# Optimization experiments

Hardware: AMD Instinct MI355X
Metric: run time of the kernel (lower is better)

## Reference

```python
import jax, jax.numpy as jnp
import numpy as np

N_CG_ITERS = 100


def _conv_same(x, k):
    # x: [C,H,W], k: [kh,kw]; depthwise cross-correlation, zero padding ('same')
    C = x.shape[0]
    rhs = jnp.broadcast_to(k, (C, 1) + k.shape)  # [C,1,kh,kw]
    return jax.lax.conv_general_dilated(
        x[None], rhs, window_strides=(1, 1), padding='SAME',
        dimension_numbers=('NCHW', 'OIHW', 'NCHW'),
        feature_group_count=C)[0]


def _flip(k):
    return k[::-1, ::-1]


def _apply_A(p, kernel, wsq, reg_kernels):
    # A = K^T K + sum_i w_i^2 G_i^T G_i
    KtKp = _conv_same(_conv_same(p, kernel), _flip(kernel))
    def one_reg(g):
        return _conv_same(_conv_same(p, g), _flip(g))
    reg = jax.vmap(one_reg)(reg_kernels)  # [n_reg, C, H, W]
    return KtKp + jnp.einsum('n,nchw->chw', wsq, reg)


def setup_inputs() -> dict:
    key = jax.random.key(0)
    k1, k2, k3, k4 = jax.random.split(key, 4)
    image = jax.random.uniform(k1, (3, 512, 512), dtype=jnp.float32)
    kernel = jax.random.uniform(k2, (11, 11), dtype=jnp.float32)
    kernel = kernel / jnp.sum(kernel)  # normalized blur PSF
    reg_kernels = 0.01 * jax.random.normal(k3, (2, 3, 3), dtype=jnp.float32)
    reg_kernel_weights = 1.0 + 0.01 * jax.random.normal(k4, (2,), dtype=jnp.float32)
    return {'image': image, 'kernel': kernel,
            'reg_kernel_weights': reg_kernel_weights, 'reg_kernels': reg_kernels}


def reference(image, kernel, reg_kernel_weights, reg_kernels):
    wsq = reg_kernel_weights * reg_kernel_weights
    # CG init: b = K^T * image, x0 = image, r0 = b - A x0, p0 = r0
    b = _conv_same(image, _flip(kernel))
    x0 = image
    r0 = b - _apply_A(x0, kernel, wsq, reg_kernels)
    p0 = r0

    def cg_step(carry, _):
        x, r, p = carry
        Ap = _apply_A(p, kernel, wsq, reg_kernels)
        rTr = jnp.sum(r * r)
        alpha = rTr / jnp.sum(p * Ap)
        x_new = x + alpha * p
        r_new = r - alpha * Ap
        beta = jnp.sum(r_new * r_new) / rTr
        p_new = r_new + beta * p
        return (x_new, r_new, p_new), None

    (x, r, p), _ = jax.lax.scan(cg_step, (x0, r0, p0), None, length=N_CG_ITERS)
    return x  # xrp[0] -> solved image [C,H,W]
```

## Files before the change

### kernel.cpp

```cpp
#include <hip/hip_runtime.h>


static constexpr int H = 512, W = 512, CCH = 3;
static constexpr int TDIM = 64;
static constexpr int RAD = 5;
static constexpr int HALO = 10;
static constexpr int PR = TDIM + 2 * HALO;
static constexpr int PSTR = 84;
static constexpr int TR = TDIM + 2 * RAD;
static constexpr int TSTR = 76;
static constexpr int NBLK = CCH * 8 * 8;
static constexpr int NTHR = 512;
static constexpr int NITER = 100;
static constexpr int FRN = 2960;
static constexpr int SPN = 2160;

__device__ __forceinline__ void load18(const float* __restrict__ row, float* __restrict__ v)
{
    const float4 a = *reinterpret_cast<const float4*>(row + 0);
    const float4 b = *reinterpret_cast<const float4*>(row + 4);
    const float4 c = *reinterpret_cast<const float4*>(row + 8);
    const float4 d = *reinterpret_cast<const float4*>(row + 12);
    const float2 e = *reinterpret_cast<const float2*>(row + 16);
    v[0]=a.x; v[1]=a.y; v[2]=a.z; v[3]=a.w;
    v[4]=b.x; v[5]=b.y; v[6]=b.z; v[7]=b.w;
    v[8]=c.x; v[9]=c.y; v[10]=c.z; v[11]=c.w;
    v[12]=d.x; v[13]=d.y; v[14]=d.z; v[15]=d.w;
    v[16]=e.x; v[17]=e.y;
}

__device__ __forceinline__ float2 allreduce2_bar(unsigned long long* slots, unsigned seq,
                                                 float va, float vb,
                                                 float* redA, float* redB, float2* bc,
                                                 int tid, int bid)
{
    __syncthreads();
    #pragma unroll
    for (int m = 32; m; m >>= 1) { va += __shfl_xor(va, m, 64); vb += __shfl_xor(vb, m, 64); }
    if ((tid & 63) == 0) { redA[tid >> 6] = va; redB[tid >> 6] = vb; }
    asm volatile("s_waitcnt vmcnt(0)" ::: "memory");
    __syncthreads();
    unsigned long long* bufA = slots + (size_t)(seq & 1u) * 512;
    unsigned long long* bufB = bufA + 256;
    if (tid == 0) {
        float sa = 0.f, sb = 0.f;
        #pragma unroll
        for (int i = 0; i < NTHR / 64; ++i) { sa += redA[i]; sb += redB[i]; }
        __hip_atomic_store(&bufA[bid],
            ((unsigned long long)seq << 32) | (unsigned long long)__float_as_uint(sa),
            __ATOMIC_RELAXED, __HIP_MEMORY_SCOPE_AGENT);
        __hip_atomic_store(&bufB[bid],
            ((unsigned long long)seq << 32) | (unsigned long long)__float_as_uint(sb),
            __ATOMIC_RELAXED, __HIP_MEMORY_SCOPE_AGENT);
    }
    float ma = 0.f, mb = 0.f;
    if (tid < NBLK) {
        unsigned long long v;
        for (;;) {
            v = __hip_atomic_load(&bufA[tid], __ATOMIC_RELAXED, __HIP_MEMORY_SCOPE_AGENT);
            if ((unsigned)(v >> 32) == seq) break;
            __builtin_amdgcn_s_sleep(1);
        }
        ma = __uint_as_float((unsigned)v);
        for (;;) {
            v = __hip_atomic_load(&bufB[tid], __ATOMIC_RELAXED, __HIP_MEMORY_SCOPE_AGENT);
            if ((unsigned)(v >> 32) == seq) break;
            __builtin_amdgcn_s_sleep(1);
        }
        mb = __uint_as_float((unsigned)v);
    }
    __syncthreads();
    #pragma unroll
    for (int m = 32; m; m >>= 1) { ma += __shfl_xor(ma, m, 64); mb += __shfl_xor(mb, m, 64); }
    if ((tid & 63) == 0) { redA[tid >> 6] = ma; redB[tid >> 6] = mb; }
    __syncthreads();
    if (tid == 0) {
        float sa = 0.f, sb = 0.f;
        #pragma unroll
        for (int i = 0; i < NTHR / 64; ++i) { sa += redA[i]; sb += redB[i]; }
        bc->x = sa; bc->y = sb;
    }
    __syncthreads();
    return *bc;
}

__device__ __forceinline__ void conv_fwd_phase(const float* __restrict__ kern,
                                               const float* __restrict__ P_,
                                               float* __restrict__ T_,
                                               int by0, int bx0, int tid)
{
    for (int seg = tid; seg < TR * 10; seg += NTHR) {
        int chunk = seg / TR;
        int ry    = seg - chunk * TR;
        int rx0   = chunk << 3;
        int gy    = by0 - RAD + ry;
        bool rowIn = (gy >= 0 && gy < H);
        float acc[8];
        #pragma unroll
        for (int j = 0; j < 8; ++j) acc[j] = 0.f;
        for (int a = 0; a < 11; ++a) {
            float v[18];
            load18(P_ + (ry + a) * PSTR + rx0, v);
            #pragma unroll
            for (int b = 0; b < 11; ++b) {
                float kw = kern[a * 11 + b];
                #pragma unroll
                for (int j = 0; j < 8; ++j) acc[j] = fmaf(v[b + j], kw, acc[j]);
            }
        }
        #pragma unroll
        for (int j = 0; j < 8; ++j) {
            int gx = bx0 - RAD + rx0 + j;
            bool in = rowIn && gx >= 0 && gx < W;
            acc[j] = in ? acc[j] : 0.f;
        }
        float* dst = T_ + ry * TSTR + rx0;
        if (rx0 < 72) {
            *reinterpret_cast<float4*>(dst)     = make_float4(acc[0], acc[1], acc[2], acc[3]);
            *reinterpret_cast<float4*>(dst + 4) = make_float4(acc[4], acc[5], acc[6], acc[7]);
        } else {
            dst[0] = acc[0];
            dst[1] = acc[1];
        }
    }
}

__device__ __forceinline__ void conv11_flip_acc_v(const float* __restrict__ src, int stride,
                                                  int row0, int col0,
                                                  const float* __restrict__ kern,
                                                  float acc[8])
{
    for (int a = 0; a < 11; ++a) {
        float v[18];
        load18(src + (row0 + a) * stride + col0, v);
        #pragma unroll
        for (int b = 0; b < 11; ++b) {
            float kw = kern[(10 - a) * 11 + (10 - b)];
            #pragma unroll
            for (int j = 0; j < 8; ++j) acc[j] = fmaf(v[b + j], kw, acc[j]);
        }
    }
}

__device__ __forceinline__ void conv11_flip_acc_s(const float* __restrict__ src, int stride,
                                                  int row0, int col0,
                                                  const float* __restrict__ kern,
                                                  float acc[8])
{
    for (int a = 0; a < 11; ++a) {
        const float* row = src + (row0 + a) * stride + col0;
        float v[18];
        #pragma unroll
        for (int b = 0; b < 18; ++b) v[b] = row[b];
        #pragma unroll
        for (int b = 0; b < 11; ++b) {
            float kw = kern[(10 - a) * 11 + (10 - b)];
            #pragma unroll
            for (int j = 0; j < 8; ++j) acc[j] = fmaf(v[b + j], kw, acc[j]);
        }
    }
}

__device__ __forceinline__ void reg_uniform(const float* __restrict__ P_,
                                            const float* __restrict__ CB_,
                                            const float* __restrict__ gk,
                                            float w0sq, float w1sq,
                                            int oy, int ox0, int gy, int gx0,
                                            float acc[8])
{
    for (int a = 0; a < 5; ++a) {
        const float* row = P_ + (oy + 8 + a) * PSTR + ox0 + 8;
        const float4 q0 = *reinterpret_cast<const float4*>(row);
        const float4 q1 = *reinterpret_cast<const float4*>(row + 4);
        const float4 q2 = *reinterpret_cast<const float4*>(row + 8);
        float v[12] = {q0.x,q0.y,q0.z,q0.w, q1.x,q1.y,q1.z,q1.w, q2.x,q2.y,q2.z,q2.w};
        #pragma unroll
        for (int b = 0; b < 5; ++b) {
            float cb = CB_[a * 5 + b];
            #pragma unroll
            for (int j = 0; j < 8; ++j) acc[j] = fmaf(v[b + j], cb, acc[j]);
        }
    }
    if (!(gy > 0 && gy < H - 1 && gx0 > 0 && gx0 + 7 < W - 1)) {
        for (int j = 0; j < 8; ++j) {
            int gx = gx0 + j;
            if (gy > 0 && gy < H - 1 && gx > 0 && gx < W - 1) continue;
            float corr = 0.f;
            for (int dy = -1; dy <= 1; ++dy)
                for (int dx = -1; dx <= 1; ++dx) {
                    int qy = gy + dy, qx = gx + dx;
                    if (qy >= 0 && qy < H && qx >= 0 && qx < W) continue;
                    float u0 = 0.f, u1 = 0.f;
                    int pr0 = oy + HALO + dy - 1, pc0 = ox0 + j + HALO + dx - 1;
                    for (int sy = 0; sy < 3; ++sy)
                        for (int sx = 0; sx < 3; ++sx) {
                            float pv = P_[(pr0 + sy) * PSTR + pc0 + sx];
                            u0 = fmaf(pv, gk[sy * 3 + sx], u0);
                            u1 = fmaf(pv, gk[9 + sy * 3 + sx], u1);
                        }
                    corr += w0sq * gk[(1 - dy) * 3 + (1 - dx)] * u0
                          + w1sq * gk[9 + (1 - dy) * 3 + (1 - dx)] * u1;
                }
            acc[j] -= corr;
        }
    }
}

__global__ void slot_init(unsigned long long* slots) { slots[threadIdx.x] = 0ull; }

__global__ void __launch_bounds__(NTHR)
deconv_cg(const float* __restrict__ img, const float* __restrict__ kern,
          const float* __restrict__ wts, const float* __restrict__ gk,
          float* __restrict__ out, float* __restrict__ ws)
{
    __shared__ alignas(16) float P[PR * PSTR + 8];
    __shared__ alignas(16) float T[TR * TSTR + 8];
    __shared__ float Sf[FRN];
    __shared__ float CB[25];
    __shared__ float redA[NTHR / 64], redB[NTHR / 64];
    __shared__ float2 bc2;

    const int tid = threadIdx.x;
    const int bid = blockIdx.x;
    const int ch  = bid / 64;
    const int tt  = bid - ch * 64;
    const int by0 = (tt >> 3) * TDIM;
    const int bx0 = (tt & 7) * TDIM;

    const float* imgc = img + ch * H * W;
    unsigned long long* slots = (unsigned long long*)ws;
    float* Hc = ws + 2048 + (size_t)ch * H * W;

    const float w0 = wts[0], w1 = wts[1];
    const float w0sq = w0 * w0, w1sq = w1 * w1;

    if (tid < 25) {
        int ty = tid / 5 - 2, tx = tid % 5 - 2;
        float s = 0.f;
        for (int ay = 0; ay < 3; ++ay)
            for (int ax = 0; ax < 3; ++ax) {
                int by_ = ay + ty, bx_ = ax + tx;
                if (by_ >= 0 && by_ < 3 && bx_ >= 0 && bx_ < 3)
                    s += w0sq * gk[ay * 3 + ax] * gk[by_ * 3 + bx_]
                       + w1sq * gk[9 + ay * 3 + ax] * gk[9 + by_ * 3 + bx_];
            }
        CB[tid] = s;
    }

    const int oy  = tid & 63;
    const int ox0 = (tid >> 6) << 3;
    const int gy  = by0 + oy;
    const int gx0 = bx0 + ox0;

    int fP[6], fG[6], fS[6];
    #pragma unroll
    for (int k = 0; k < 6; ++k) {
        int idx = tid + k * NTHR;
        fP[k] = -1; fG[k] = -1; fS[k] = idx;
        if (idx < FRN) {
            int py, px;
            if (idx < 840)       { py = idx / 84;              px = idx - py * 84; }
            else if (idx < 1680) { int t = idx - 840;  py = 74 + t / 84; px = t - (t / 84) * 84; }
            else                 { int t = idx - 1680; py = 10 + t / 20;
                                   int c = t - (t / 20) * 20;  px = (c < 10) ? c : (c + 64); }
            int iy = by0 - HALO + py, ix = bx0 - HALO + px;
            if (iy >= 0 && iy < H && ix >= 0 && ix < W) {
                fP[k] = py * PSTR + px;
                fG[k] = iy * W + ix;
            }
        }
    }
    int pT[5], pG[5];
    #pragma unroll
    for (int k = 0; k < 5; ++k) {
        int idx = tid + k * NTHR;
        pT[k] = -1; pG[k] = 0;
        if (idx < SPN) {
            int sy, sx;
            if (idx < 640)       { sy = idx >> 6;              sx = idx & 63; }
            else if (idx < 1280) { int t = idx - 640;  sy = 54 + (t >> 6); sx = t & 63; }
            else                 { int t = idx - 1280; sy = 10 + t / 20;
                                   int c = t - (t / 20) * 20;  sx = (c < 10) ? c : (c + 44); }
            pT[k] = sy * TSTR + sx;
            pG[k] = (by0 + sy) * W + bx0 + sx;
        }
    }

    float xr[8], rr[8], pr[8], sr[8];
    #pragma unroll
    for (int j = 0; j < 8; ++j) { pr[j] = 0.f; sr[j] = 0.f; }
    for (int idx = tid; idx < FRN; idx += NTHR) Sf[idx] = 0.f;

    for (int idx = tid; idx < PR * PR; idx += NTHR) {
        int py = idx / PR, px = idx - py * PR;
        int iy = by0 - HALO + py, ix = bx0 - HALO + px;
        float v = 0.f;
        if (iy >= 0 && iy < H && ix >= 0 && ix < W) v = imgc[iy * W + ix];
        P[py * PSTR + px] = v;
    }
    __syncthreads();
    conv_fwd_phase(kern, P, T, by0, bx0, tid);
    __syncthreads();
    {
        float accA[8], accB[8];
        #pragma unroll
        for (int j = 0; j < 8; ++j) { accA[j] = 0.f; accB[j] = 0.f; }
        conv11_flip_acc_v(T, TSTR, oy, ox0, kern, accA);
        conv11_flip_acc_s(P, PSTR, oy + 5, ox0 + 5, kern, accB);
        reg_uniform(P, CB, gk, w0sq, w1sq, oy, ox0, gy, gx0, accA);
        #pragma unroll
        for (int j = 0; j < 8; ++j) {
            rr[j] = accB[j] - accA[j];
            xr[j] = P[(oy + HALO) * PSTR + ox0 + HALO + j];
        }
        __syncthreads();
        float* st = T + oy * TSTR + ox0;
        *reinterpret_cast<float4*>(st)     = make_float4(rr[0], rr[1], rr[2], rr[3]);
        *reinterpret_cast<float4*>(st + 4) = make_float4(rr[4], rr[5], rr[6], rr[7]);
        __syncthreads();
        #pragma unroll
        for (int k = 0; k < 5; ++k)
            if (pT[k] >= 0)
                __hip_atomic_store(&Hc[pG[k]], T[pT[k]],
                                   __ATOMIC_RELAXED, __HIP_MEMORY_SCOPE_AGENT);
        (void)allreduce2_bar(slots, 1u, 0.f, 0.f, redA, redB, &bc2, tid, bid);
        #pragma unroll
        for (int k = 0; k < 6; ++k)
            if (fG[k] >= 0)
                P[fP[k]] = __hip_atomic_load(&Hc[fG[k]],
                                             __ATOMIC_RELAXED, __HIP_MEMORY_SCOPE_AGENT);
        float* ow = P + (oy + HALO) * PSTR + ox0 + HALO;
        *reinterpret_cast<float2*>(ow)     = make_float2(rr[0], rr[1]);
        *reinterpret_cast<float2*>(ow + 2) = make_float2(rr[2], rr[3]);
        *reinterpret_cast<float2*>(ow + 4) = make_float2(rr[4], rr[5]);
        *reinterpret_cast<float2*>(ow + 6) = make_float2(rr[6], rr[7]);
    }

    float gamma_old = 1.f, alpha_old = 1.f;

    for (int it = 0; it < NITER; ++it) {
        __syncthreads();

        conv_fwd_phase(kern, P, T, by0, bx0, tid);
        __syncthreads();
        float wv[8];
        float ga = 0.f, de = 0.f;
        {
            float acc[8];
            #pragma unroll
            for (int j = 0; j < 8; ++j) acc[j] = 0.f;
            conv11_flip_acc_v(T, TSTR, oy, ox0, kern, acc);
            reg_uniform(P, CB, gk, w0sq, w1sq, oy, ox0, gy, gx0, acc);
            #pragma unroll
            for (int j = 0; j < 8; ++j) {
                wv[j] = acc[j];
                ga = fmaf(rr[j], rr[j], ga);
                de = fmaf(rr[j], wv[j], de);
            }
        }
        __syncthreads();
        float* st = T + oy * TSTR + ox0;
        *reinterpret_cast<float4*>(st)     = make_float4(wv[0], wv[1], wv[2], wv[3]);
        *reinterpret_cast<float4*>(st + 4) = make_float4(wv[4], wv[5], wv[6], wv[7]);
        __syncthreads();
        #pragma unroll
        for (int k = 0; k < 5; ++k)
            if (pT[k] >= 0)
                __hip_atomic_store(&Hc[pG[k]], T[pT[k]],
                                   __ATOMIC_RELAXED, __HIP_MEMORY_SCOPE_AGENT);

        float2 gd = allreduce2_bar(slots, (unsigned)(it + 2), ga, de,
                                   redA, redB, &bc2, tid, bid);
        float gamma = gd.x, delta = gd.y;
        float beta  = (it == 0) ? 0.f : gamma / gamma_old;
        float alpha = (it == 0) ? gamma / delta
                                : gamma / (delta - beta * gamma / alpha_old);

        float wf[6];
        #pragma unroll
        for (int k = 0; k < 6; ++k)
            wf[k] = (fG[k] >= 0)
                  ? __hip_atomic_load(&Hc[fG[k]], __ATOMIC_RELAXED, __HIP_MEMORY_SCOPE_AGENT)
                  : 0.f;

        #pragma unroll
        for (int j = 0; j < 8; ++j) {
            pr[j] = fmaf(beta, pr[j], rr[j]);
            sr[j] = fmaf(beta, sr[j], wv[j]);
            xr[j] = fmaf(alpha, pr[j], xr[j]);
            rr[j] = fmaf(-alpha, sr[j], rr[j]);
        }
        #pragma unroll
        for (int k = 0; k < 6; ++k)
            if (fG[k] >= 0) {
                float s = fmaf(beta, Sf[fS[k]], wf[k]);
                Sf[fS[k]] = s;
                P[fP[k]]  = fmaf(-alpha, s, P[fP[k]]);
            }
        float* ow = P + (oy + HALO) * PSTR + ox0 + HALO;
        *reinterpret_cast<float2*>(ow)     = make_float2(rr[0], rr[1]);
        *reinterpret_cast<float2*>(ow + 2) = make_float2(rr[2], rr[3]);
        *reinterpret_cast<float2*>(ow + 4) = make_float2(rr[4], rr[5]);
        *reinterpret_cast<float2*>(ow + 6) = make_float2(rr[6], rr[7]);

        gamma_old = gamma;
        alpha_old = alpha;
    }

    float* op = out + ch * H * W + gy * W + gx0;
    *reinterpret_cast<float4*>(op)     = make_float4(xr[0], xr[1], xr[2], xr[3]);
    *reinterpret_cast<float4*>(op + 4) = make_float4(xr[4], xr[5], xr[6], xr[7]);
}

extern "C" void kernel_launch(void* const* d_in, const int* in_sizes, int n_in,
                              void* d_out, int out_size, void* d_ws, size_t ws_size,
                              hipStream_t stream)
{
    (void)in_sizes; (void)n_in; (void)out_size; (void)ws_size;
    const float* img  = (const float*)d_in[0];
    const float* kern = (const float*)d_in[1];
    const float* wts  = (const float*)d_in[2];
    const float* gk   = (const float*)d_in[3];
    float* out = (float*)d_out;
    float* ws  = (float*)d_ws;

    slot_init<<<1, 1024, 0, stream>>>((unsigned long long*)ws);
    deconv_cg<<<dim3(NBLK), dim3(NTHR), 0, stream>>>(img, kern, wts, gk, out, ws);
}
```

Measured before the change: 4.207 ms.

## Centralize grid allreduce in block zero and broadcast result via flag slots

The grid-wide two-value allreduce used to have every block poll all 192 per-block slots and reduce them itself. Now only block 0 gathers and reduces the partial sums and publishes the two totals to dedicated result slots, which every other block polls with a single thread. This cuts global polling traffic and redundant reductions across blocks, but adds a second serialized hop through block 0 and lengthens the critical path. The workspace offset is moved to make room for the new result slots, and slot_init zeroes them.

After: 4.565 ms. 1.08x slower.

```diff
diff --git a/kernel.cpp b/kernel.cpp
--- a/kernel.cpp
+++ b/kernel.cpp
@@ -42,6 +42,7 @@
     __syncthreads();
     unsigned long long* bufA = slots + (size_t)(seq & 1u) * 512;
     unsigned long long* bufB = bufA + 256;
+    unsigned long long* res  = slots + 1024 + (size_t)(seq & 1u) * 8;
     if (tid == 0) {
         float sa = 0.f, sb = 0.f;
         #pragma unroll
@@ -53,32 +54,54 @@
             ((unsigned long long)seq << 32) | (unsigned long long)__float_as_uint(sb),
             __ATOMIC_RELAXED, __HIP_MEMORY_SCOPE_AGENT);
     }
-    float ma = 0.f, mb = 0.f;
-    if (tid < NBLK) {
+    if (bid == 0) {
+        float ma = 0.f, mb = 0.f;
+        if (tid < NBLK) {
+            unsigned long long v;
+            for (;;) {
+                v = __hip_atomic_load(&bufA[tid], __ATOMIC_RELAXED, __HIP_MEMORY_SCOPE_AGENT);
+                if ((unsigned)(v >> 32) == seq) break;
+                __builtin_amdgcn_s_sleep(1);
+            }
+            ma = __uint_as_float((unsigned)v);
+            for (;;) {
+                v = __hip_atomic_load(&bufB[tid], __ATOMIC_RELAXED, __HIP_MEMORY_SCOPE_AGENT);
+                if ((unsigned)(v >> 32) == seq) break;
+                __builtin_amdgcn_s_sleep(1);
+            }
+            mb = __uint_as_float((unsigned)v);
+        }
+        __syncthreads();
+        #pragma unroll
+        for (int m = 32; m; m >>= 1) { ma += __shfl_xor(ma, m, 64); mb += __shfl_xor(mb, m, 64); }
+        if ((tid & 63) == 0) { redA[tid >> 6] = ma; redB[tid >> 6] = mb; }
+        __syncthreads();
+        if (tid == 0) {
+            float g = 0.f, d = 0.f;
+            #pragma unroll
+            for (int i = 0; i < NTHR / 64; ++i) { g += redA[i]; d += redB[i]; }
+            __hip_atomic_store(&res[0],
+                ((unsigned long long)seq << 32) | (unsigned long long)__float_as_uint(g),
+                __ATOMIC_RELAXED, __HIP_MEMORY_SCOPE_AGENT);
+            __hip_atomic_store(&res[1],
+                ((unsigned long long)seq << 32) | (unsigned long long)__float_as_uint(d),
+                __ATOMIC_RELAXED, __HIP_MEMORY_SCOPE_AGENT);
+        }
+    }
+    if (tid == 0) {
         unsigned long long v;
         for (;;) {
-            v = __hip_atomic_load(&bufA[tid], __ATOMIC_RELAXED, __HIP_MEMORY_SCOPE_AGENT);
+            v = __hip_atomic_load(&res[0], __ATOMIC_RELAXED, __HIP_MEMORY_SCOPE_AGENT);
             if ((unsigned)(v >> 32) == seq) break;
             __builtin_amdgcn_s_sleep(1);
         }
-        ma = __uint_as_float((unsigned)v);
+        bc->x = __uint_as_float((unsigned)v);
         for (;;) {
-            v = __hip_atomic_load(&bufB[tid], __ATOMIC_RELAXED, __HIP_MEMORY_SCOPE_AGENT);
+            v = __hip_atomic_load(&res[1], __ATOMIC_RELAXED, __HIP_MEMORY_SCOPE_AGENT);
             if ((unsigned)(v >> 32) == seq) break;
             __builtin_amdgcn_s_sleep(1);
         }
-        mb = __uint_as_float((unsigned)v);
-    }
-    __syncthreads();
-    #pragma unroll
-    for (int m = 32; m; m >>= 1) { ma += __shfl_xor(ma, m, 64); mb += __shfl_xor(mb, m, 64); }
-    if ((tid & 63) == 0) { redA[tid >> 6] = ma; redB[tid >> 6] = mb; }
-    __syncthreads();
-    if (tid == 0) {
-        float sa = 0.f, sb = 0.f;
-        #pragma unroll
-        for (int i = 0; i < NTHR / 64; ++i) { sa += redA[i]; sb += redB[i]; }
-        bc->x = sa; bc->y = sb;
+        bc->y = __uint_as_float((unsigned)v);
     }
     __syncthreads();
     return *bc;
@@ -206,7 +229,11 @@
     }
 }
 
-__global__ void slot_init(unsigned long long* slots) { slots[threadIdx.x] = 0ull; }
+__global__ void slot_init(unsigned long long* slots)
+{
+    slots[threadIdx.x] = 0ull;
+    slots[threadIdx.x + 1024] = 0ull;
+}
 
 __global__ void __launch_bounds__(NTHR)
 deconv_cg(const float* __restrict__ img, const float* __restrict__ kern,
@@ -229,7 +256,7 @@
 
     const float* imgc = img + ch * H * W;
     unsigned long long* slots = (unsigned long long*)ws;
-    float* Hc = ws + 2048 + (size_t)ch * H * W;
+    float* Hc = ws + 4096 + (size_t)ch * H * W;
 
     const float w0 = wts[0], w1 = wts[1];
     const float w0sq = w0 * w0, w1sq = w1 * w1;
```

## Double block threads so forward conv runs in one pass with 740 threads

Applied to the files above, without the earlier changes.

Raises the block size from 512 to 1024 threads. All 740 forward-conv row segments now run in a single pass instead of two strided passes, which removes the tail imbalance. Only the first 512 threads own output pixels for the adjoint conv and the CG vector updates. Halo exchange and frame updates are spread over more threads, so each thread does fewer items. The cost is higher register pressure under the 1024-thread launch bound, and idle threads during the owner-only phases.

Result: slower. 8.075 ms (+91.9%).

```diff
diff --git a/kernel.cpp b/kernel.cpp
--- a/kernel.cpp
+++ b/kernel.cpp
@@ -10,7 +10,8 @@
 static constexpr int TR = TDIM + 2 * RAD;
 static constexpr int TSTR = 76;
 static constexpr int NBLK = CCH * 8 * 8;
-static constexpr int NTHR = 512;
+static constexpr int NTHR = 1024;
+static constexpr int NOWN = 512;
 static constexpr int NITER = 100;
 static constexpr int FRN = 2960;
 static constexpr int SPN = 2160;
@@ -89,39 +90,39 @@
                                                float* __restrict__ T_,
                                                int by0, int bx0, int tid)
 {
-    for (int seg = tid; seg < TR * 10; seg += NTHR) {
-        int chunk = seg / TR;
-        int ry    = seg - chunk * TR;
-        int rx0   = chunk << 3;
-        int gy    = by0 - RAD + ry;
-        bool rowIn = (gy >= 0 && gy < H);
-        float acc[8];
-        #pragma unroll
-        for (int j = 0; j < 8; ++j) acc[j] = 0.f;
-        for (int a = 0; a < 11; ++a) {
-            float v[18];
-            load18(P_ + (ry + a) * PSTR + rx0, v);
-            #pragma unroll
-            for (int b = 0; b < 11; ++b) {
-                float kw = kern[a * 11 + b];
-                #pragma unroll
-                for (int j = 0; j < 8; ++j) acc[j] = fmaf(v[b + j], kw, acc[j]);
-            }
-        }
-        #pragma unroll
-        for (int j = 0; j < 8; ++j) {
-            int gx = bx0 - RAD + rx0 + j;
-            bool in = rowIn && gx >= 0 && gx < W;
-            acc[j] = in ? acc[j] : 0.f;
-        }
-        float* dst = T_ + ry * TSTR + rx0;
-        if (rx0 < 72) {
-            *reinterpret_cast<float4*>(dst)     = make_float4(acc[0], acc[1], acc[2], acc[3]);
-            *reinterpret_cast<float4*>(dst + 4) = make_float4(acc[4], acc[5], acc[6], acc[7]);
-        } else {
-            dst[0] = acc[0];
-            dst[1] = acc[1];
-        }
+    if (tid >= 740) return;
+    int chunk, ry;
+    if (tid < 640) { chunk = tid >> 6; ry = tid & 63; }
+    else { int u = tid - 640; chunk = u / 10; ry = 64 + (u - 10 * (u / 10)); }
+    const int rx0 = chunk << 3;
+    const int gy  = by0 - RAD + ry;
+    const bool rowIn = (gy >= 0 && gy < H);
+    float acc[8];
+    #pragma unroll
+    for (int j = 0; j < 8; ++j) acc[j] = 0.f;
+    for (int a = 0; a < 11; ++a) {
+        float v[18];
+        load18(P_ + (ry + a) * PSTR + rx0, v);
+        #pragma unroll
+        for (int b = 0; b < 11; ++b) {
+            float kw = kern[a * 11 + b];
+            #pragma unroll
+            for (int j = 0; j < 8; ++j) acc[j] = fmaf(v[b + j], kw, acc[j]);
+        }
+    }
+    #pragma unroll
+    for (int j = 0; j < 8; ++j) {
+        int gx = bx0 - RAD + rx0 + j;
+        bool in = rowIn && gx >= 0 && gx < W;
+        acc[j] = in ? acc[j] : 0.f;
+    }
+    float* dst = T_ + ry * TSTR + rx0;
+    if (rx0 < 72) {
+        *reinterpret_cast<float4*>(dst)     = make_float4(acc[0], acc[1], acc[2], acc[3]);
+        *reinterpret_cast<float4*>(dst + 4) = make_float4(acc[4], acc[5], acc[6], acc[7]);
+    } else {
+        dst[0] = acc[0];
+        dst[1] = acc[1];
     }
 }
 
@@ -226,6 +227,7 @@
     const int tt  = bid - ch * 64;
     const int by0 = (tt >> 3) * TDIM;
     const int bx0 = (tt & 7) * TDIM;
+    const bool own = (tid < NOWN);
 
     const float* imgc = img + ch * H * W;
     unsigned long long* slots = (unsigned long long*)ws;
@@ -248,13 +250,13 @@
     }
 
     const int oy  = tid & 63;
-    const int ox0 = (tid >> 6) << 3;
+    const int ox0 = ((tid >> 6) & 7) << 3;
     const int gy  = by0 + oy;
     const int gx0 = bx0 + ox0;
 
-    int fP[6], fG[6], fS[6];
-    #pragma unroll
-    for (int k = 0; k < 6; ++k) {
+    int fP[3], fG[3], fS[3];
+    #pragma unroll
+    for (int k = 0; k < 3; ++k) {
         int idx = tid + k * NTHR;
         fP[k] = -1; fG[k] = -1; fS[k] = idx;
         if (idx < FRN) {
@@ -270,9 +272,9 @@
             }
         }
     }
-    int pT[5], pG[5];
-    #pragma unroll
-    for (int k = 0; k < 5; ++k) {
+    int pT[3], pG[3];
+    #pragma unroll
+    for (int k = 0; k < 3; ++k) {
         int idx = tid + k * NTHR;
         pT[k] = -1; pG[k] = 0;
         if (idx < SPN) {
@@ -288,7 +290,7 @@
 
     float xr[8], rr[8], pr[8], sr[8];
     #pragma unroll
-    for (int j = 0; j < 8; ++j) { pr[j] = 0.f; sr[j] = 0.f; }
+    for (int j = 0; j < 8; ++j) { pr[j] = 0.f; sr[j] = 0.f; rr[j] = 0.f; xr[j] = 0.f; }
     for (int idx = tid; idx < FRN; idx += NTHR) Sf[idx] = 0.f;
 
     for (int idx = tid; idx < PR * PR; idx += NTHR) {
@@ -301,7 +303,7 @@
     __syncthreads();
     conv_fwd_phase(kern, P, T, by0, bx0, tid);
     __syncthreads();
-    {
+    if (own) {
         float accA[8], accB[8];
         #pragma unroll
         for (int j = 0; j < 8; ++j) { accA[j] = 0.f; accB[j] = 0.f; }
@@ -313,22 +315,26 @@
             rr[j] = accB[j] - accA[j];
             xr[j] = P[(oy + HALO) * PSTR + ox0 + HALO + j];
         }
-        __syncthreads();
+    }
+    __syncthreads();
+    if (own) {
         float* st = T + oy * TSTR + ox0;
         *reinterpret_cast<float4*>(st)     = make_float4(rr[0], rr[1], rr[2], rr[3]);
         *reinterpret_cast<float4*>(st + 4) = make_float4(rr[4], rr[5], rr[6], rr[7]);
-        __syncthreads();
-        #pragma unroll
-        for (int k = 0; k < 5; ++k)
-            if (pT[k] >= 0)
-                __hip_atomic_store(&Hc[pG[k]], T[pT[k]],
-                                   __ATOMIC_RELAXED, __HIP_MEMORY_SCOPE_AGENT);
-        (void)allreduce2_bar(slots, 1u, 0.f, 0.f, redA, redB, &bc2, tid, bid);
-        #pragma unroll
-        for (int k = 0; k < 6; ++k)
-            if (fG[k] >= 0)
-                P[fP[k]] = __hip_atomic_load(&Hc[fG[k]],
-                                             __ATOMIC_RELAXED, __HIP_MEMORY_SCOPE_AGENT);
+    }
+    __syncthreads();
+    #pragma unroll
+    for (int k = 0; k < 3; ++k)
+        if (pT[k] >= 0)
+            __hip_atomic_store(&Hc[pG[k]], T[pT[k]],
+                               __ATOMIC_RELAXED, __HIP_MEMORY_SCOPE_AGENT);
+    (void)allreduce2_bar(slots, 1u, 0.f, 0.f, redA, redB, &bc2, tid, bid);
+    #pragma unroll
+    for (int k = 0; k < 3; ++k)
+        if (fG[k] >= 0)
+            P[fP[k]] = __hip_atomic_load(&Hc[fG[k]],
+                                         __ATOMIC_RELAXED, __HIP_MEMORY_SCOPE_AGENT);
+    if (own) {
         float* ow = P + (oy + HALO) * PSTR + ox0 + HALO;
         *reinterpret_cast<float2*>(ow)     = make_float2(rr[0], rr[1]);
         *reinterpret_cast<float2*>(ow + 2) = make_float2(rr[2], rr[3]);
@@ -345,7 +351,9 @@
         __syncthreads();
         float wv[8];
         float ga = 0.f, de = 0.f;
-        {
+        #pragma unroll
+        for (int j = 0; j < 8; ++j) wv[j] = 0.f;
+        if (own) {
             float acc[8];
             #pragma unroll
             for (int j = 0; j < 8; ++j) acc[j] = 0.f;
@@ -359,12 +367,14 @@
             }
         }
         __syncthreads();
-        float* st = T + oy * TSTR + ox0;
-        *reinterpret_cast<float4*>(st)     = make_float4(wv[0], wv[1], wv[2], wv[3]);
-        *reinterpret_cast<float4*>(st + 4) = make_float4(wv[4], wv[5], wv[6], wv[7]);
+        if (own) {
+            float* st = T + oy * TSTR + ox0;
+            *reinterpret_cast<float4*>(st)     = make_float4(wv[0], wv[1], wv[2], wv[3]);
+            *reinterpret_cast<float4*>(st + 4) = make_float4(wv[4], wv[5], wv[6], wv[7]);
+        }
         __syncthreads();
         #pragma unroll
-        for (int k = 0; k < 5; ++k)
+        for (int k = 0; k < 3; ++k)
             if (pT[k] >= 0)
                 __hip_atomic_store(&Hc[pG[k]], T[pT[k]],
                                    __ATOMIC_RELAXED, __HIP_MEMORY_SCOPE_AGENT);
@@ -376,40 +386,46 @@
         float alpha = (it == 0) ? gamma / delta
                                 : gamma / (delta - beta * gamma / alpha_old);
 
-        float wf[6];
-        #pragma unroll
-        for (int k = 0; k < 6; ++k)
+        float wf[3];
+        #pragma unroll
+        for (int k = 0; k < 3; ++k)
             wf[k] = (fG[k] >= 0)
                   ? __hip_atomic_load(&Hc[fG[k]], __ATOMIC_RELAXED, __HIP_MEMORY_SCOPE_AGENT)
                   : 0.f;
 
-        #pragma unroll
-        for (int j = 0; j < 8; ++j) {
-            pr[j] = fmaf(beta, pr[j], rr[j]);
-            sr[j] = fmaf(beta, sr[j], wv[j]);
-            xr[j] = fmaf(alpha, pr[j], xr[j]);
-            rr[j] = fmaf(-alpha, sr[j], rr[j]);
-        }
-        #pragma unroll
-        for (int k = 0; k < 6; ++k)
+        if (own) {
+            #pragma unroll
+            for (int j = 0; j < 8; ++j) {
+                pr[j] = fmaf(beta, pr[j], rr[j]);
+                sr[j] = fmaf(beta, sr[j], wv[j]);
+                xr[j] = fmaf(alpha, pr[j], xr[j]);
+                rr[j] = fmaf(-alpha, sr[j], rr[j]);
+            }
+        }
+        #pragma unroll
+        for (int k = 0; k < 3; ++k)
             if (fG[k] >= 0) {
                 float s = fmaf(beta, Sf[fS[k]], wf[k]);
                 Sf[fS[k]] = s;
                 P[fP[k]]  = fmaf(-alpha, s, P[fP[k]]);
             }
-        float* ow = P + (oy + HALO) * PSTR + ox0 + HALO;
-        *reinterpret_cast<float2*>(ow)     = make_float2(rr[0], rr[1]);
-        *reinterpret_cast<float2*>(ow + 2) = make_float2(rr[2], rr[3]);
-        *reinterpret_cast<float2*>(ow + 4) = make_float2(rr[4], rr[5]);
-        *reinterpret_cast<float2*>(ow + 6) = make_float2(rr[6], rr[7]);
+        if (own) {
+            float* ow = P + (oy + HALO) * PSTR + ox0 + HALO;
+            *reinterpret_cast<float2*>(ow)     = make_float2(rr[0], rr[1]);
+            *reinterpret_cast<float2*>(ow + 2) = make_float2(rr[2], rr[3]);
+            *reinterpret_cast<float2*>(ow + 4) = make_float2(rr[4], rr[5]);
+            *reinterpret_cast<float2*>(ow + 6) = make_float2(rr[6], rr[7]);
+        }
 
         gamma_old = gamma;
         alpha_old = alpha;
     }
 
-    float* op = out + ch * H * W + gy * W + gx0;
-    *reinterpret_cast<float4*>(op)     = make_float4(xr[0], xr[1], xr[2], xr[3]);
-    *reinterpret_cast<float4*>(op + 4) = make_float4(xr[4], xr[5], xr[6], xr[7]);
+    if (own) {
+        float* op = out + ch * H * W + gy * W + gx0;
+        *reinterpret_cast<float4*>(op)     = make_float4(xr[0], xr[1], xr[2], xr[3]);
+        *reinterpret_cast<float4*>(op + 4) = make_float4(xr[4], xr[5], xr[6], xr[7]);
+    }
 }
 
 extern "C" void kernel_launch(void* const* d_in, const int* in_sizes, int n_in,
```
